# Kernel optimization log

Hardware: AMD Instinct MI355X
Metric: run time of the kernel (lower is better)

Reference implementation:

```python
import math
import jax, jax.numpy as jnp
from jax import lax
import numpy as np

B, HH, WW = 8, 128, 128
N = HH * WW
DIM, NH = 256, 4
HD = DIM // 2 // NH          # 32, per-head dim of the halved channels
CH = DIM // 2                # 128
THETA, MAXSEQ = 10000.0, 4096

# --- static FoPE frequency setup (mirrors RotaryEmbedding.get_inv_freq with fope=True) ---
def _inv_freq():
    rot = 2 * HD                                   # rotary dim = d_model//n_heads = 2*head_dim
    inv = 1.0 / THETA ** (np.arange(0, rot, 2, dtype=np.float64) / rot)
    return inv[inv >= 2.0 * np.pi / MAXSEQ].astype(np.float32)

INV_FREQ = _inv_freq()
D_IN = int(INV_FREQ.shape[0])                      # 23
D_OUT = D_IN if D_IN <= (2 * HD) // 4 else (2 * HD) // 4   # 16


def _coef(key, gain=0.5):
    # xavier_normal_ on (NH, D_IN, D_OUT) + step-eye offset, as in FourierEmbedding.__init__
    fan_in, fan_out = D_IN * D_OUT, NH * D_OUT
    std = gain * math.sqrt(2.0 / (fan_in + fan_out))
    c = std * jax.random.normal(key, (NH, D_IN, D_OUT), jnp.float32)
    step = math.ceil(D_IN / D_OUT)
    eye = np.zeros((NH, D_IN, D_OUT), np.float32)
    for i in range(D_OUT):
        if i * step < D_IN:
            eye[:, i * step, i] = 1.0
    return c + jnp.asarray(eye)


def setup_inputs() -> dict:
    key = jax.random.key(0)
    ks = jax.random.split(key, 10)
    def lin(k, o, i):
        lim = 1.0 / math.sqrt(i)
        return jax.random.uniform(k, (o, i), jnp.float32, -lim, lim)
    return {
        "x": jax.random.normal(ks[0], (B, N, DIM), jnp.float32),
        "Wq": lin(ks[1], CH, DIM), "bq": jnp.zeros((CH,), jnp.float32),
        "Wk": lin(ks[2], CH, DIM), "bk": jnp.zeros((CH,), jnp.float32),
        "Wv": lin(ks[3], CH, DIM), "bv": jnp.zeros((CH,), jnp.float32),
        # Hedgehog maps init as identity
        "Whq": jnp.eye(HD, dtype=jnp.float32), "bhq": jnp.zeros((HD,), jnp.float32),
        "Whk": jnp.eye(HD, dtype=jnp.float32), "bhk": jnp.zeros((HD,), jnp.float32),
        "sin_coef": _coef(ks[4]), "cos_coef": _coef(ks[5]),
        "lepe_w": 0.02 * jax.random.normal(ks[6], (CH, 1, 3, 3), jnp.float32),
        "lepe_b": jnp.zeros((CH,), jnp.float32),
        "temperature": jnp.ones((CH, 1), jnp.float32),
        "Wp": lin(ks[7], DIM, DIM), "bp": jnp.zeros((DIM,), jnp.float32),
        "h": HH, "w": WW,
    }


def _hedgehog(t, W, b):
    # t: [b,h,n,HD] -> [b,h,n,2*HD]
    y = jnp.einsum('bhnd,ed->bhne', t, W) + b
    return jax.nn.softmax(jnp.concatenate([2.0 * y, -2.0 * y], axis=-1), axis=-1)


def _fope(t, sin_coef, cos_coef, n):
    # t: [b,h,n,2*HD]; learnable Fourier rotary
    freqs = jnp.arange(n, dtype=jnp.float32)[:, None] * jnp.asarray(INV_FREQ)[None, :]  # [n,D_IN]
    cs = sin_coef / sin_coef.sum(axis=-2, keepdims=True)
    cc = cos_coef / cos_coef.sum(axis=-2, keepdims=True)
    fs = jnp.einsum('tD,hDd->htd', jnp.sin(freqs), cs)[None]   # [1,h,n,D_OUT]
    fc = jnp.einsum('tD,hDd->htd', jnp.cos(freqs), cc)[None]
    pad = ((0, 0), (0, 0), (0, 0), (0, HD - D_OUT))
    fs = jnp.pad(fs, pad, constant_values=1.0)
    fc = jnp.pad(fc, pad, constant_values=1.0)
    fs = jnp.concatenate([fs, fs], axis=-1)                    # [1,h,n,2*HD]
    fc = jnp.concatenate([fc, fc], axis=-1)
    x1, x2 = t[..., :HD], t[..., HD:]
    rot = jnp.concatenate([-x2, x1], axis=-1)
    return t * fc - rot * fs


def _forward(x, Wq, bq, Wk, bk, Wv, bv, Whq, bhq, Whk, bhk,
             sin_coef, cos_coef, lepe_w, lepe_b, temperature, Wp, bp, h, w):
    b, n, _ = x.shape
    q = x @ Wq.T + bq   # [b,n,CH]
    k = x @ Wk.T + bk
    v = x @ Wv.T + bv

    # ---- spatial brand (Hedgehog linear attention with Fourier rotary) ----
    qh = q.reshape(b, n, NH, HD).swapaxes(1, 2)   # [b,nh,n,HD]
    kh = k.reshape(b, n, NH, HD).swapaxes(1, 2)
    vh = v.reshape(b, n, NH, HD).swapaxes(1, 2)
    qf = _hedgehog(qh, Whq, bhq)                  # [b,nh,n,2HD]
    kf = _hedgehog(kh, Whk, bhk)
    q_fope = _fope(qf, sin_coef, cos_coef, n)
    k_fope = _fope(kf, sin_coef, cos_coef, n)
    kmean = kf.mean(axis=-2, keepdims=True)                       # [b,nh,1,2HD]
    z = 1.0 / (jnp.einsum('bhnd,bhsd->bhns', qf, kmean) + 1e-6)   # [b,nh,n,1]
    s = n ** (-0.5)
    kv = jnp.einsum('bhnd,bhne->bhde', k_fope * s, vh * s)        # [b,nh,2HD,HD]
    xs = jnp.einsum('bhnd,bhde->bhne', q_fope, kv) * z            # [b,nh,n,HD]
    xs = xs.swapaxes(1, 2).reshape(b, n, CH)
    v_img = vh.swapaxes(-1, -2).reshape(b, CH, h, w)
    conv = lax.conv_general_dilated(v_img, lepe_w, (1, 1), 'SAME',
                                    feature_group_count=CH,
                                    dimension_numbers=('NCHW', 'OIHW', 'NCHW'))
    conv = conv + lepe_b[None, :, None, None]
    x_spatial = conv.reshape(b, CH, n).transpose(0, 2, 1) + xs    # [b,n,CH]

    # ---- channel brand (transposed attention over channels) ----
    qc = q.swapaxes(-1, -2)   # [b,CH,n]
    kc = k.swapaxes(-1, -2)
    vc = v.swapaxes(-1, -2)
    qn = qc / jnp.maximum(jnp.linalg.norm(qc, axis=-1, keepdims=True), 1e-12)
    kn = kc / jnp.maximum(jnp.linalg.norm(kc, axis=-1, keepdims=True), 1e-12)
    attn = jax.nn.softmax(jnp.einsum('bcl,bdl->bcd', qn, kn) * temperature, axis=-1)
    x_channel = jnp.einsum('bcd,bdl->bcl', attn, vc).swapaxes(-1, -2)  # [b,n,CH]

    out = jnp.concatenate([x_spatial, x_channel], axis=-1) @ Wp.T + bp  # [b,n,DIM]
    return out, q, k


def reference(x, Wq, bq, Wk, bk, Wv, bv, Whq, bhq, Whk, bhk,
              sin_coef, cos_coef, lepe_w, lepe_b, temperature, Wp, bp, h, w):
    return _forward(x, Wq, bq, Wk, bk, Wv, bv, Whq, bhq, Whk, bhk,
                    sin_coef, cos_coef, lepe_w, lepe_b, temperature, Wp, bp, h, w)
```

## Files before the change

kernel.cpp:

```cpp
#include <hip/hip_runtime.h>
#include <cmath>

#define NB 8
#define NN 16384
#define DIN 23
#define DOUT 16

typedef short bf16x8 __attribute__((ext_vector_type(8)));
typedef float f32x4 __attribute__((ext_vector_type(4)));

__device__ __forceinline__ unsigned short f2bf(float f) {
    unsigned int u = __float_as_uint(f);
    u += 0x7FFFu + ((u >> 16) & 1u);
    return (unsigned short)(u >> 16);
}
__device__ __forceinline__ float bf2f(unsigned short s) {
    return __uint_as_float(((unsigned int)s) << 16);
}
__device__ __forceinline__ float rcpf(float x) { return __builtin_amdgcn_rcpf(x); }

__device__ __forceinline__ bf16x8 cvt8(float4 a, float4 b) {
    bf16x8 r;
    r[0]=(short)f2bf(a.x); r[1]=(short)f2bf(a.y); r[2]=(short)f2bf(a.z); r[3]=(short)f2bf(a.w);
    r[4]=(short)f2bf(b.x); r[5]=(short)f2bf(b.y); r[6]=(short)f2bf(b.z); r[7]=(short)f2bf(b.w);
    return r;
}
__device__ __forceinline__ void red16(f32x4& s) {
    #pragma unroll
    for (int off = 1; off < 16; off <<= 1) {
        s[0] += __shfl_xor(s[0], off); s[1] += __shfl_xor(s[1], off);
        s[2] += __shfl_xor(s[2], off); s[3] += __shfl_xor(s[3], off);
    }
}
__device__ __forceinline__ void red16x2(f32x4& s, f32x4& w) {
    #pragma unroll
    for (int off = 1; off < 16; off <<= 1) {
        s[0] += __shfl_xor(s[0], off); s[1] += __shfl_xor(s[1], off);
        s[2] += __shfl_xor(s[2], off); s[3] += __shfl_xor(s[3], off);
        w[0] += __shfl_xor(w[0], off); w[1] += __shfl_xor(w[1], off);
        w[2] += __shfl_xor(w[2], off); w[3] += __shfl_xor(w[3], off);
    }
}

#define WS_XSPB   ((size_t)0)
#define WS_G      ((size_t)8388608)
#define WS_VB     ((size_t)16777216)
#define WS_XSB    ((size_t)25165824)
#define WS_FS     ((size_t)33554432)
#define WS_INV    ((size_t)35651584)
#define WS_CS     ((size_t)35651648)
#define WS_CC     ((size_t)35653184)
#define WS_WCAT   ((size_t)35654720)
#define WS_BCAT   ((size_t)35703872)
#define WS_KVPART ((size_t)35704256)
#define WS_KMPART ((size_t)37801408)
#define WS_KV     ((size_t)37866944)
#define WS_KMEAN  ((size_t)37932480)
#define WS_QN2    ((size_t)37934528)
#define WS_KN2    ((size_t)37935552)
#define WS_ATTN   ((size_t)38067648)
#define WS_BMATT  ((size_t)38198720)
#define WS_QB     ((size_t)38460864)
#define WS_KB     ((size_t)46849472)

__global__ __launch_bounds__(256) void k_wprep(
    const float* __restrict__ Wq, const float* __restrict__ Wk, const float* __restrict__ Wv,
    const float* __restrict__ bq, const float* __restrict__ bk, const float* __restrict__ bv,
    const float* __restrict__ sc, const float* __restrict__ ccin,
    unsigned short* __restrict__ Wc, float* __restrict__ bcat,
    float* __restrict__ inv, float* __restrict__ cs, float* __restrict__ cc)
{
    int row = blockIdx.x, t = threadIdx.x;
    if (row == 384) {
        if (t >= 64) return;
        if (t < DIN) inv[t] = (float)pow(10000.0, -((double)(2 * t)) / 64.0);
        int h = t >> 4, d = t & 15;
        float ss = 0.f, s2 = 0.f;
        for (int D = 0; D < DIN; ++D) { ss += sc[(h*DIN + D)*DOUT + d]; s2 += ccin[(h*DIN + D)*DOUT + d]; }
        float rs = 1.f / ss, r2 = 1.f / s2;
        for (int D = 0; D < DIN; ++D) {
            cs[(h*DIN + D)*DOUT + d] = sc[(h*DIN + D)*DOUT + d] * rs;
            cc[(h*DIN + D)*DOUT + d] = ccin[(h*DIN + D)*DOUT + d] * r2;
        }
        return;
    }
    const float* W = (row < 128) ? Wq : (row < 256) ? Wk : Wv;
    const float* bb = (row < 128) ? bq : (row < 256) ? bk : bv;
    int r = row & 127;
    Wc[(size_t)row*256 + t] = f2bf(W[(size_t)r*256 + t]);
    if (t == 0) bcat[row] = bb[r];
}

__global__ __launch_bounds__(256) void k_tables(const float* __restrict__ inv, const float* __restrict__ cs,
                                                const float* __restrict__ cc,
                                                unsigned int* __restrict__ fsc)
{
    int t = threadIdx.x;
    int sub = t >> 6, lane = t & 63;
    int tpos = blockIdx.x*4 + sub;
    __shared__ float ssin[4][DIN], scos[4][DIN];
    if (lane < DIN) { float fr = (float)tpos * inv[lane]; ssin[sub][lane] = sinf(fr); scos[sub][lane] = cosf(fr); }
    __syncthreads();
    int h = lane >> 4, d = lane & 15;
    float as = 0.f, ac = 0.f;
    for (int D = 0; D < DIN; ++D) { as += ssin[sub][D]*cs[(h*DIN + D)*DOUT + d]; ac += scos[sub][D]*cc[(h*DIN + D)*DOUT + d]; }
    fsc[((size_t)h*NN + tpos)*16 + d] = ((unsigned int)f2bf(ac) << 16) | (unsigned int)f2bf(as);
}

__global__ __launch_bounds__(512) void k_qkv_mfma(const float* __restrict__ x,
    const unsigned short* __restrict__ Wc, const float* __restrict__ bcat,
    float* __restrict__ q, float* __restrict__ k,
    unsigned short* __restrict__ qb, unsigned short* __restrict__ kb,
    unsigned short* __restrict__ vb)
{
    __shared__ __align__(16) char smem[65536];
    int t = threadIdx.x;
    int lin = blockIdx.x;
    int mtile = (lin & 7)*128 + (lin >> 3);
    int m0 = mtile * 128;
    int wave = t >> 6, lane = t & 63;
    int wm = wave >> 2, wn = wave & 3;
    int lrow = lane & 15, lk = lane >> 4;
    f32x4 acc[4][6];
    #pragma unroll
    for (int i = 0; i < 4; ++i)
        #pragma unroll
        for (int j = 0; j < 6; ++j) acc[i][j] = (f32x4){0.f,0.f,0.f,0.f};

    int am = t >> 4, ak4 = t & 15;
    size_t arow = (size_t)(m0 + am);
    float4 pa[4];
    #pragma unroll
    for (int p = 0; p < 4; ++p)
        pa[p] = *reinterpret_cast<const float4*>(&x[(arow + p*32)*256 + ak4*4]);

    #pragma unroll
    for (int kt = 0; kt < 4; ++kt) {
        int k0 = kt * 64;
        if (kt) __syncthreads();
        #pragma unroll
        for (int p = 0; p < 4; ++p) {
            int m = am + p*32;
            ushort4 b4;
            b4.x = f2bf(pa[p].x); b4.y = f2bf(pa[p].y); b4.z = f2bf(pa[p].z); b4.w = f2bf(pa[p].w);
            int byte = m*128 + ((ak4*8) ^ ((m & 7) << 4));
            *reinterpret_cast<ushort4*>(smem + byte) = b4;
        }
        {
            int n = t >> 3, k8 = t & 7;
            #pragma unroll
            for (int p = 0; p < 6; ++p, n += 64) {
                uint4 u4 = *reinterpret_cast<const uint4*>(&Wc[(size_t)n*256 + k0 + k8*8]);
                int byte = n*128 + ((k8 ^ (n & 7)) << 4);
                *reinterpret_cast<uint4*>(smem + 16384 + byte) = u4;
            }
        }
        if (kt < 3) {
            #pragma unroll
            for (int p = 0; p < 4; ++p)
                pa[p] = *reinterpret_cast<const float4*>(&x[(arow + p*32)*256 + (kt+1)*64 + ak4*4]);
        }
        __syncthreads();
        #pragma unroll
        for (int ks = 0; ks < 2; ++ks) {
            bf16x8 af[4];
            #pragma unroll
            for (int mi = 0; mi < 4; ++mi) {
                int m = wm*64 + mi*16 + lrow;
                int u = (ks*4 + lk) ^ (m & 7);
                af[mi] = *reinterpret_cast<const bf16x8*>(smem + m*128 + u*16);
            }
            #pragma unroll
            for (int ni = 0; ni < 6; ++ni) {
                int n = wn*96 + ni*16 + lrow;
                int u = (ks*4 + lk) ^ (n & 7);
                bf16x8 bfv = *reinterpret_cast<const bf16x8*>(smem + 16384 + n*128 + u*16);
                #pragma unroll
                for (int mi = 0; mi < 4; ++mi)
                    acc[mi][ni] = __builtin_amdgcn_mfma_f32_16x16x32_bf16(af[mi], bfv, acc[mi][ni], 0, 0, 0);
            }
        }
    }
    #pragma unroll
    for (int mi = 0; mi < 4; ++mi) {
        #pragma unroll
        for (int ni = 0; ni < 6; ++ni) {
            int gcol = wn*96 + ni*16 + lrow;
            int c = gcol & 127;
            float bias = bcat[gcol];
            #pragma unroll
            for (int r = 0; r < 4; ++r) {
                size_t grow = (size_t)m0 + wm*64 + mi*16 + lk*4 + r;
                float val = acc[mi][ni][r] + bias;
                if (gcol < 128)      { __builtin_nontemporal_store(val, &q[grow*128 + c]); qb[grow*128 + c] = f2bf(val); }
                else if (gcol < 256) { __builtin_nontemporal_store(val, &k[grow*128 + c]); kb[grow*128 + c] = f2bf(val); }
                else                 vb[grow*128 + c] = f2bf(val);
            }
        }
    }
}

__global__ __launch_bounds__(256) void k_conv(const unsigned short* __restrict__ vb, const float* __restrict__ w,
                                              const float* __restrict__ bias, unsigned short* __restrict__ xspb)
{
    __shared__ float wsmT[9][128];
    __shared__ float bsm[128];
    int t = threadIdx.x;
    for (int i = t; i < 1152; i += 256) wsmT[i % 9][i / 9] = w[i];
    if (t < 128) bsm[t] = bias[t];
    __syncthreads();
    int jj = t >> 4, c8 = (t & 15) * 8;
    int j = blockIdx.x * 16 + jj;
    int i = blockIdx.y, b = blockIdx.z;
    float acc[8];
    #pragma unroll
    for (int l = 0; l < 8; ++l) acc[l] = bsm[c8 + l];
    #pragma unroll
    for (int di = 0; di < 3; ++di) {
        int ii = i + di - 1;
        if (ii < 0 || ii >= 128) continue;
        #pragma unroll
        for (int dj = 0; dj < 3; ++dj) {
            int jx = j + dj - 1;
            if (jx < 0 || jx >= 128) continue;
            uint4 u = *reinterpret_cast<const uint4*>(&vb[((size_t)b*NN + ii*128 + jx)*128 + c8]);
            const unsigned short* us = (const unsigned short*)&u;
            int kk = di*3 + dj;
            #pragma unroll
            for (int l = 0; l < 8; ++l)
                acc[l] += wsmT[kk][c8 + l] * bf2f(us[l]);
        }
    }
    ushort4 r0, r1;
    r0.x = f2bf(acc[0]); r0.y = f2bf(acc[1]); r0.z = f2bf(acc[2]); r0.w = f2bf(acc[3]);
    r1.x = f2bf(acc[4]); r1.y = f2bf(acc[5]); r1.z = f2bf(acc[6]); r1.w = f2bf(acc[7]);
    size_t ob = ((size_t)b*NN + i*128 + j)*128 + c8;
    *reinterpret_cast<ushort4*>(&xspb[ob]) = r0;
    *reinterpret_cast<ushort4*>(&xspb[ob+4]) = r1;
}

__global__ __launch_bounds__(256) void k_featkv(
    const unsigned short* __restrict__ kb, const unsigned short* __restrict__ vb,
    const float* __restrict__ W, const float* __restrict__ bvec,
    const unsigned int* __restrict__ fsc,
    float* __restrict__ kvpart, float* __restrict__ kmpart)
{
    __shared__ __align__(16) char smem[34816];
    __shared__ float kms[4][64];
    int bh = blockIdx.y, b = bh >> 2, h = bh & 3;
    int chunk = blockIdx.x;
    int t = threadIdx.x, w = t >> 6, lane = t & 63;
    int c = lane & 15, g = lane >> 4;
    unsigned short* kfsTw = reinterpret_cast<unsigned short*>(smem) + w*2560;
    unsigned short* vTw   = reinterpret_cast<unsigned short*>(smem + 20480) + w*1280;
    bf16x8 wb[2];
    #pragma unroll
    for (int et = 0; et < 2; ++et) {
        float4 wa = *reinterpret_cast<const float4*>(&W[(c + et*16)*32 + g*8]);
        float4 wb2 = *reinterpret_cast<const float4*>(&W[(c + et*16)*32 + g*8 + 4]);
        wb[et] = cvt8(wa, wb2);
    }
    float bias0 = bvec[c], bias1 = bvec[c + 16];
    f32x4 acc[4][2];
    #pragma unroll
    for (int i = 0; i < 4; ++i) { acc[i][0] = (f32x4){0.f,0.f,0.f,0.f}; acc[i][1] = (f32x4){0.f,0.f,0.f,0.f}; }
    f32x4 km0 = {0.f,0.f,0.f,0.f}, km1 = km0, km2 = km0, km3 = km0;

    for (int rnd = 0; rnd < 4; ++rnd) {
        int p0 = chunk*512 + w*128 + rnd*32;
        {
            uint4 vr0, vr1;
            size_t vbase = ((size_t)(b*NN + p0 + c*2))*128 + h*32 + g*8;
            vr0 = *reinterpret_cast<const uint4*>(&vb[vbase]);
            vr1 = *reinterpret_cast<const uint4*>(&vb[vbase + 128]);
            #pragma unroll
            for (int j = 0; j < 8; ++j) {
                ushort2 pk;
                pk.x = ((const unsigned short*)&vr0)[j];
                pk.y = ((const unsigned short*)&vr1)[j];
                *reinterpret_cast<ushort2*>(&vTw[(g*8 + j)*40 + c*2]) = pk;
            }
        }
        #pragma unroll
        for (int mt = 0; mt < 2; ++mt) {
            int posA = p0 + mt*16 + c;
            bf16x8 af = *reinterpret_cast<const bf16x8*>(&kb[((size_t)(b*NN + posA))*128 + h*32 + g*8]);
            f32x4 z4 = {0.f,0.f,0.f,0.f};
            f32x4 y0 = __builtin_amdgcn_mfma_f32_16x16x32_bf16(af, wb[0], z4, 0, 0, 0);
            f32x4 y1 = __builtin_amdgcn_mfma_f32_16x16x32_bf16(af, wb[1], z4, 0, 0, 0);
            f32x4 el0, eh0, el1, eh1;
            #pragma unroll
            for (int r = 0; r < 4; ++r) {
                float a0 = 2.f*(y0[r] + bias0);
                float a1 = 2.f*(y1[r] + bias1);
                el0[r] = __expf(a0); eh0[r] = __expf(-a0);
                el1[r] = __expf(a1); eh1[r] = __expf(-a1);
            }
            f32x4 s = el0 + eh0 + el1 + eh1;
            red16(s);
            f32x4 rs;
            #pragma unroll
            for (int r = 0; r < 4; ++r) rs[r] = rcpf(s[r]);
            f32x4 klo0 = el0*rs, khi0 = eh0*rs, klo1 = el1*rs, khi1 = eh1*rs;
            km0 += klo0; km1 += khi0; km2 += klo1; km3 += khi1;
            int posC = p0 + mt*16 + g*4;
            ushort4 wlo0, whi0, wlo1, whi1;
            #pragma unroll
            for (int r = 0; r < 4; ++r) {
                unsigned int u = fsc[((size_t)h*NN + posC + r)*16 + c];
                float fsv = bf2f((unsigned short)(u & 0xffffu));
                float fcv = bf2f((unsigned short)(u >> 16));
                ((unsigned short*)&wlo0)[r] = f2bf(klo0[r]*fcv + khi0[r]*fsv);
                ((unsigned short*)&whi0)[r] = f2bf(khi0[r]*fcv - klo0[r]*fsv);
                ((unsigned short*)&wlo1)[r] = f2bf(klo1[r] + khi1[r]);
                ((unsigned short*)&whi1)[r] = f2bf(khi1[r] - klo1[r]);
            }
            int po = mt*16 + g*4;
            *reinterpret_cast<ushort4*>(&kfsTw[(c)*40 + po])      = wlo0;
            *reinterpret_cast<ushort4*>(&kfsTw[(32 + c)*40 + po]) = whi0;
            *reinterpret_cast<ushort4*>(&kfsTw[(16 + c)*40 + po]) = wlo1;
            *reinterpret_cast<ushort4*>(&kfsTw[(48 + c)*40 + po]) = whi1;
        }
        {
            bf16x8 bf0 = *reinterpret_cast<const bf16x8*>(&vTw[(c)*40 + g*8]);
            bf16x8 bf1 = *reinterpret_cast<const bf16x8*>(&vTw[(16 + c)*40 + g*8]);
            #pragma unroll
            for (int mt = 0; mt < 4; ++mt) {
                bf16x8 af2 = *reinterpret_cast<const bf16x8*>(&kfsTw[(mt*16 + c)*40 + g*8]);
                acc[mt][0] = __builtin_amdgcn_mfma_f32_16x16x32_bf16(af2, bf0, acc[mt][0], 0, 0, 0);
                acc[mt][1] = __builtin_amdgcn_mfma_f32_16x16x32_bf16(af2, bf1, acc[mt][1], 0, 0, 0);
            }
        }
    }
    float kv0 = km0[0]+km0[1]+km0[2]+km0[3];
    float kv1 = km1[0]+km1[1]+km1[2]+km1[3];
    float kv2 = km2[0]+km2[1]+km2[2]+km2[3];
    float kv3 = km3[0]+km3[1]+km3[2]+km3[3];
    kv0 += __shfl_xor(kv0, 16); kv0 += __shfl_xor(kv0, 32);
    kv1 += __shfl_xor(kv1, 16); kv1 += __shfl_xor(kv1, 32);
    kv2 += __shfl_xor(kv2, 16); kv2 += __shfl_xor(kv2, 32);
    kv3 += __shfl_xor(kv3, 16); kv3 += __shfl_xor(kv3, 32);
    if (g == 0) {
        kms[w][c] = kv0; kms[w][16 + c] = kv2; kms[w][32 + c] = kv1; kms[w][48 + c] = kv3;
    }
    __syncthreads();
    float* kvred = reinterpret_cast<float*>(smem);
    #pragma unroll
    for (int mt = 0; mt < 4; ++mt)
        #pragma unroll
        for (int nt = 0; nt < 2; ++nt) {
            int d = nt*16 + c;
            *reinterpret_cast<f32x4*>(&kvred[(size_t)(w*32 + d)*68 + mt*16 + g*4]) = acc[mt][nt];
        }
    __syncthreads();
    #pragma unroll
    for (int i = 0; i < 8; ++i) {
        int idx = t*8 + i;
        int f = idx >> 5, d = idx & 31;
        float s2 = kvred[(0*32 + d)*68 + f] + kvred[(1*32 + d)*68 + f]
                 + kvred[(2*32 + d)*68 + f] + kvred[(3*32 + d)*68 + f];
        kvpart[((size_t)(bh*32 + chunk))*2048 + idx] = s2;
    }
    if (t < 64) {
        float s2 = kms[0][t] + kms[1][t] + kms[2][t] + kms[3][t];
        kmpart[(size_t)(bh*32 + chunk)*64 + t] = s2;
    }
}

__global__ __launch_bounds__(256) void k_kvred2(const float* __restrict__ kvpart, const float* __restrict__ kmpart,
                                                unsigned short* __restrict__ kvT, float* __restrict__ kmean)
{
    int bh = blockIdx.x >> 3, part = blockIdx.x & 7;
    int idx = part*256 + threadIdx.x;
    float s = 0.f;
    for (int cidx = 0; cidx < 32; ++cidx) s += kvpart[((size_t)(bh*32 + cidx))*2048 + idx];
    int f = idx >> 5, d = idx & 31;
    kvT[(size_t)bh*2048 + d*64 + f] = f2bf(s * (1.f/16384.f));
    if (part == 0 && threadIdx.x < 64) {
        int tt = threadIdx.x;
        float sm = 0.f;
        for (int cidx = 0; cidx < 32; ++cidx) sm += kmpart[(size_t)(bh*32 + cidx)*64 + tt];
        kmean[bh*64 + tt] = sm * (1.f/16384.f);
    }
}

__global__ __launch_bounds__(256) void k_featxs(
    const unsigned short* __restrict__ qb, const float* __restrict__ W, const float* __restrict__ bvec,
    const unsigned int* __restrict__ fsc, const unsigned short* __restrict__ kvT,
    const float* __restrict__ kmean, const unsigned short* __restrict__ xspb, unsigned short* __restrict__ xsb)
{
    __shared__ __align__(16) unsigned short qfs[4][32][72];
    int bh = blockIdx.y, b = bh >> 2, h = bh & 3;
    int chunk = blockIdx.x;
    int t = threadIdx.x, w = t >> 6, lane = t & 63;
    int c = lane & 15, g = lane >> 4;
    bf16x8 wb[2];
    #pragma unroll
    for (int et = 0; et < 2; ++et) {
        float4 wa = *reinterpret_cast<const float4*>(&W[(c + et*16)*32 + g*8]);
        float4 wb2 = *reinterpret_cast<const float4*>(&W[(c + et*16)*32 + g*8 + 4]);
        wb[et] = cvt8(wa, wb2);
    }
    float bias0 = bvec[c], bias1 = bvec[c + 16];
    float kml0 = kmean[bh*64 + c],      kml1 = kmean[bh*64 + 16 + c];
    float kmh0 = kmean[bh*64 + 32 + c], kmh1 = kmean[bh*64 + 48 + c];
    bf16x8 bkv[2][2];
    #pragma unroll
    for (int nt = 0; nt < 2; ++nt)
        #pragma unroll
        for (int ks = 0; ks < 2; ++ks)
            bkv[nt][ks] = *reinterpret_cast<const bf16x8*>(&kvT[(size_t)bh*2048 + (nt*16 + c)*64 + ks*32 + g*8]);

    for (int rnd = 0; rnd < 2; ++rnd) {
        int p0 = chunk*256 + w*64 + rnd*32;
        #pragma unroll
        for (int mt = 0; mt < 2; ++mt) {
            int posA = p0 + mt*16 + c;
            bf16x8 af = *reinterpret_cast<const bf16x8*>(&qb[((size_t)(b*NN + posA))*128 + h*32 + g*8]);
            f32x4 z4 = {0.f,0.f,0.f,0.f};
            f32x4 y0 = __builtin_amdgcn_mfma_f32_16x16x32_bf16(af, wb[0], z4, 0, 0, 0);
            f32x4 y1 = __builtin_amdgcn_mfma_f32_16x16x32_bf16(af, wb[1], z4, 0, 0, 0);
            f32x4 el0, eh0, el1, eh1;
            #pragma unroll
            for (int r = 0; r < 4; ++r) {
                float a0 = 2.f*(y0[r] + bias0);
                float a1 = 2.f*(y1[r] + bias1);
                el0[r] = __expf(a0); eh0[r] = __expf(-a0);
                el1[r] = __expf(a1); eh1[r] = __expf(-a1);
            }
            f32x4 s = el0 + eh0 + el1 + eh1;
            f32x4 wv = el0*kml0 + eh0*kmh0 + el1*kml1 + eh1*kmh1;
            red16x2(s, wv);
            f32x4 zr;
            #pragma unroll
            for (int r = 0; r < 4; ++r) {
                float rs = rcpf(s[r]);
                float z = rcpf(wv[r]*rs + 1e-6f);
                zr[r] = z*rs;
            }
            int posC = mt*16 + g*4;
            #pragma unroll
            for (int r = 0; r < 4; ++r) {
                unsigned int u = fsc[((size_t)h*NN + p0 + posC + r)*16 + c];
                float fsv = bf2f((unsigned short)(u & 0xffffu));
                float fcv = bf2f((unsigned short)(u >> 16));
                qfs[w][posC + r][c]      = f2bf(zr[r]*(el0[r]*fcv + eh0[r]*fsv));
                qfs[w][posC + r][32 + c] = f2bf(zr[r]*(eh0[r]*fcv - el0[r]*fsv));
                qfs[w][posC + r][16 + c] = f2bf(zr[r]*(el1[r] + eh1[r]));
                qfs[w][posC + r][48 + c] = f2bf(zr[r]*(eh1[r] - el1[r]));
            }
        }
        f32x4 acc[2][2];
        #pragma unroll
        for (int i = 0; i < 2; ++i) { acc[i][0] = (f32x4){0.f,0.f,0.f,0.f}; acc[i][1] = (f32x4){0.f,0.f,0.f,0.f}; }
        #pragma unroll
        for (int ks = 0; ks < 2; ++ks)
            #pragma unroll
            for (int mt = 0; mt < 2; ++mt) {
                bf16x8 af2 = *reinterpret_cast<const bf16x8*>(&qfs[w][mt*16 + c][ks*32 + g*8]);
                acc[mt][0] = __builtin_amdgcn_mfma_f32_16x16x32_bf16(af2, bkv[0][ks], acc[mt][0], 0, 0, 0);
                acc[mt][1] = __builtin_amdgcn_mfma_f32_16x16x32_bf16(af2, bkv[1][ks], acc[mt][1], 0, 0, 0);
            }
        #pragma unroll
        for (int mt = 0; mt < 2; ++mt)
            #pragma unroll
            for (int nt = 0; nt < 2; ++nt) {
                int d = nt*16 + c;
                #pragma unroll
                for (int r = 0; r < 4; ++r) {
                    int pos = p0 + mt*16 + g*4 + r;
                    size_t off = ((size_t)(b*NN + pos))*128 + h*32 + d;
                    xsb[off] = f2bf(bf2f(xspb[off]) + acc[mt][nt][r]);
                }
            }
    }
}

__global__ __launch_bounds__(256) void k_gram(const unsigned short* __restrict__ qb, const unsigned short* __restrict__ kb,
                                              float* __restrict__ G,
                                              float* __restrict__ qn2, float* __restrict__ kn2)
{
    __shared__ unsigned short qTs[128][40];
    __shared__ unsigned short kTs[128][40];
    int kc = blockIdx.x, bb = blockIdx.y;
    int t = threadIdx.x, lane = t & 63;
    int wave = t >> 6, wm = wave >> 1, wn = wave & 1;
    int c = t & 127, lh = t >> 7;
    float qa = 0.f, ka = 0.f;
    f32x4 acc[4][4];
    #pragma unroll
    for (int i = 0; i < 4; ++i)
        #pragma unroll
        for (int j = 0; j < 4; ++j) acc[i][j] = (f32x4){0.f,0.f,0.f,0.f};

    for (int kt = 0; kt < 16; ++kt) {
        __syncthreads();
        #pragma unroll
        for (int i = 0; i < 16; ++i) {
            int l = lh*16 + i;
            size_t pos = (size_t)bb*NN + kc*512 + kt*32 + l;
            unsigned short qu = qb[pos*128 + c];
            unsigned short ku = kb[pos*128 + c];
            float qv = bf2f(qu), kvv = bf2f(ku);
            qa += qv*qv; ka += kvv*kvv;
            qTs[c][l] = qu;
            kTs[c][l] = ku;
        }
        __syncthreads();
        bf16x8 af[4];
        #pragma unroll
        for (int mi = 0; mi < 4; ++mi)
            af[mi] = *reinterpret_cast<const bf16x8*>(&qTs[wm*64 + mi*16 + (lane & 15)][(lane >> 4)*8]);
        #pragma unroll
        for (int ni = 0; ni < 4; ++ni) {
            bf16x8 bfr = *reinterpret_cast<const bf16x8*>(&kTs[wn*64 + ni*16 + (lane & 15)][(lane >> 4)*8]);
            #pragma unroll
            for (int mi = 0; mi < 4; ++mi)
                acc[mi][ni] = __builtin_amdgcn_mfma_f32_16x16x32_bf16(af[mi], bfr, acc[mi][ni], 0, 0, 0);
        }
    }
    #pragma unroll
    for (int mi = 0; mi < 4; ++mi) {
        #pragma unroll
        for (int ni = 0; ni < 4; ++ni) {
            int d = wn*64 + ni*16 + (lane & 15);
            #pragma unroll
            for (int r = 0; r < 4; ++r) {
                int cc = wm*64 + mi*16 + (lane >> 4)*4 + r;
                atomicAdd(&G[(size_t)bb*16384 + (size_t)cc*128 + d], acc[mi][ni][r]);
            }
        }
    }
    atomicAdd(&qn2[bb*128 + c], qa);
    atomicAdd(&kn2[bb*128 + c], ka);
}

__global__ __launch_bounds__(128) void k_attnsm(const float* __restrict__ G, const float* __restrict__ qn2,
    const float* __restrict__ kn2, const float* __restrict__ temp, float* __restrict__ attn)
{
    __shared__ float red[128];
    int row = blockIdx.x;
    int b = row >> 7, c = row & 127;
    int t = threadIdx.x;
    float s0 = G[(size_t)b*16384 + (size_t)c*128 + t];
    float qn = fmaxf(sqrtf(qn2[b*128 + c]), 1e-12f);
    float kn = fmaxf(sqrtf(kn2[b*128 + t]), 1e-12f);
    float val = s0 / (qn*kn) * temp[c];
    red[t] = val; __syncthreads();
    for (int s = 64; s > 0; s >>= 1) { if (t < s) red[t] = fmaxf(red[t], red[t+s]); __syncthreads(); }
    float mm = red[0]; __syncthreads();
    float ev = expf(val - mm);
    red[t] = ev; __syncthreads();
    for (int s = 64; s > 0; s >>= 1) { if (t < s) red[t] += red[t+s]; __syncthreads(); }
    attn[(size_t)row*128 + t] = ev / red[0];
}

__global__ __launch_bounds__(256) void k_bmat(const float* __restrict__ attn, const float* __restrict__ Wp,
                                              unsigned short* __restrict__ BmatT)
{
    int b = blockIdx.y, kk = blockIdx.x, o = threadIdx.x;
    float val;
    if (kk < 128) {
        val = Wp[(size_t)o*256 + kk];
    } else {
        int d = kk - 128;
        __shared__ float a[128];
        if (o < 128) a[o] = attn[((size_t)b*128 + o)*128 + d];
        __syncthreads();
        float acc = 0.f;
        for (int c = 0; c < 128; ++c) acc += a[c] * Wp[(size_t)o*256 + 128 + c];
        val = acc;
    }
    BmatT[((size_t)b*256 + o)*256 + kk] = f2bf(val);
}

__global__ __launch_bounds__(256) void k_out_mfma(const unsigned short* __restrict__ xsb,
    const unsigned short* __restrict__ vb, const unsigned short* __restrict__ BmatT,
    const float* __restrict__ bp, float* __restrict__ out)
{
    __shared__ unsigned short Asm[128*64];
    __shared__ unsigned short Bsm[128*64];
    int t = threadIdx.x;
    int lin = blockIdx.y*2 + blockIdx.x;
    int logical = (lin & 7)*256 + (lin >> 3);
    int ntile = logical & 1;
    int mtile = logical >> 1;
    int m0 = mtile * 128;
    int n0 = ntile * 128;
    int b = mtile >> 7;
    int wave = t >> 6, lane = t & 63;
    int wm = wave >> 1, wn = wave & 1;
    int lrow = lane & 15, lk = lane >> 4;
    f32x4 acc[4][4];
    #pragma unroll
    for (int i = 0; i < 4; ++i)
        #pragma unroll
        for (int j = 0; j < 4; ++j) acc[i][j] = (f32x4){0.f,0.f,0.f,0.f};

    int am = t >> 3, ak8 = t & 7;
    uint4 pa4[4];
    #pragma unroll
    for (int p = 0; p < 4; ++p)
        pa4[p] = *reinterpret_cast<const uint4*>(&xsb[(size_t)(m0 + am + p*32)*128 + ak8*8]);

    #pragma unroll
    for (int kt = 0; kt < 4; ++kt) {
        if (kt) __syncthreads();
        #pragma unroll
        for (int p = 0; p < 4; ++p) {
            int m = am + p*32;
            int byte = m*128 + ((ak8 ^ (m & 7)) << 4);
            *reinterpret_cast<uint4*>(reinterpret_cast<char*>(Asm) + byte) = pa4[p];
        }
        {
            int n = t >> 3, k8 = t & 7;
            #pragma unroll
            for (int p = 0; p < 4; ++p, n += 32) {
                uint4 u4 = *reinterpret_cast<const uint4*>(&BmatT[((size_t)b*256 + n0 + n)*256 + kt*64 + k8*8]);
                int byte = n*128 + ((k8 ^ (n & 7)) << 4);
                *reinterpret_cast<uint4*>(reinterpret_cast<char*>(Bsm) + byte) = u4;
            }
        }
        if (kt < 3) {
            const unsigned short* Asrc = ((kt+1) < 2) ? xsb : vb;
            int ka0 = ((kt+1) & 1) * 64;
            #pragma unroll
            for (int p = 0; p < 4; ++p)
                pa4[p] = *reinterpret_cast<const uint4*>(&Asrc[(size_t)(m0 + am + p*32)*128 + ka0 + ak8*8]);
        }
        __syncthreads();
        #pragma unroll
        for (int ks = 0; ks < 2; ++ks) {
            bf16x8 af[4], bfv[4];
            #pragma unroll
            for (int mi = 0; mi < 4; ++mi) {
                int m = wm*64 + mi*16 + lrow;
                int u = (ks*4 + lk) ^ (m & 7);
                af[mi] = *reinterpret_cast<const bf16x8*>(reinterpret_cast<const char*>(Asm) + m*128 + u*16);
            }
            #pragma unroll
            for (int ni = 0; ni < 4; ++ni) {
                int n = wn*64 + ni*16 + lrow;
                int u = (ks*4 + lk) ^ (n & 7);
                bfv[ni] = *reinterpret_cast<const bf16x8*>(reinterpret_cast<const char*>(Bsm) + n*128 + u*16);
            }
            #pragma unroll
            for (int mi = 0; mi < 4; ++mi)
                #pragma unroll
                for (int ni = 0; ni < 4; ++ni)
                    acc[mi][ni] = __builtin_amdgcn_mfma_f32_16x16x32_bf16(af[mi], bfv[ni], acc[mi][ni], 0, 0, 0);
        }
    }
    #pragma unroll
    for (int mi = 0; mi < 4; ++mi) {
        #pragma unroll
        for (int ni = 0; ni < 4; ++ni) {
            int gcol = n0 + wn*64 + ni*16 + lrow;
            float bias = bp[gcol];
            #pragma unroll
            for (int r = 0; r < 4; ++r) {
                size_t grow = (size_t)m0 + wm*64 + mi*16 + lk*4 + r;
                __builtin_nontemporal_store(acc[mi][ni][r] + bias, &out[grow*256 + gcol]);
            }
        }
    }
}

extern "C" void kernel_launch(void* const* d_in, const int* in_sizes, int n_in,
                              void* d_out, int out_size, void* d_ws, size_t ws_size,
                              hipStream_t stream)
{
    (void)in_sizes; (void)n_in; (void)out_size; (void)ws_size;
    const float* x    = (const float*)d_in[0];
    const float* Wq   = (const float*)d_in[1];
    const float* bq   = (const float*)d_in[2];
    const float* Wk   = (const float*)d_in[3];
    const float* bk   = (const float*)d_in[4];
    const float* Wv   = (const float*)d_in[5];
    const float* bv   = (const float*)d_in[6];
    const float* Whq  = (const float*)d_in[7];
    const float* bhq  = (const float*)d_in[8];
    const float* Whk  = (const float*)d_in[9];
    const float* bhk  = (const float*)d_in[10];
    const float* sinc = (const float*)d_in[11];
    const float* cosc = (const float*)d_in[12];
    const float* lw   = (const float*)d_in[13];
    const float* lb   = (const float*)d_in[14];
    const float* temp = (const float*)d_in[15];
    const float* Wp   = (const float*)d_in[16];
    const float* bp   = (const float*)d_in[17];

    float* out = (float*)d_out;
    float* q   = out + 33554432;
    float* k   = out + 50331648;
    float* ws  = (float*)d_ws;

    unsigned short* xspb = (unsigned short*)(ws + WS_XSPB);
    float* G      = ws + WS_G;
    unsigned short* vbuf = (unsigned short*)(ws + WS_VB);
    unsigned short* xsb  = (unsigned short*)(ws + WS_XSB);
    unsigned int* fsc = (unsigned int*)(ws + WS_FS);
    float* inv    = ws + WS_INV;
    float* cs     = ws + WS_CS;
    float* cc     = ws + WS_CC;
    unsigned short* Wc = (unsigned short*)(ws + WS_WCAT);
    float* bcat   = ws + WS_BCAT;
    float* kvpart = ws + WS_KVPART;
    float* kmpart = ws + WS_KMPART;
    unsigned short* kvT = (unsigned short*)(ws + WS_KV);
    float* kmean  = ws + WS_KMEAN;
    float* qn2    = ws + WS_QN2;
    float* kn2    = ws + WS_KN2;
    float* attn   = ws + WS_ATTN;
    unsigned short* BmatT = (unsigned short*)(ws + WS_BMATT);
    unsigned short* qbuf  = (unsigned short*)(ws + WS_QB);
    unsigned short* kbuf  = (unsigned short*)(ws + WS_KB);

    hipMemsetAsync(qn2, 0, 2048*sizeof(float), stream);
    hipMemsetAsync(G, 0, 131072*sizeof(float), stream);

    k_wprep<<<385, 256, 0, stream>>>(Wq, Wk, Wv, bq, bk, bv, sinc, cosc, Wc, bcat, inv, cs, cc);
    k_tables<<<4096, 256, 0, stream>>>(inv, cs, cc, fsc);
    k_qkv_mfma<<<1024, 512, 0, stream>>>(x, Wc, bcat, q, k, qbuf, kbuf, vbuf);
    k_conv<<<dim3(8, 128, 8), 256, 0, stream>>>(vbuf, lw, lb, xspb);
    k_featkv<<<dim3(32, 32), 256, 0, stream>>>(kbuf, vbuf, Whk, bhk, fsc, kvpart, kmpart);
    k_kvred2<<<256, 256, 0, stream>>>(kvpart, kmpart, kvT, kmean);
    k_featxs<<<dim3(64, 32), 256, 0, stream>>>(qbuf, Whq, bhq, fsc, kvT, kmean, xspb, xsb);
    k_gram<<<dim3(32, 8), 256, 0, stream>>>(qbuf, kbuf, G, qn2, kn2);
    k_attnsm<<<1024, 128, 0, stream>>>(G, qn2, kn2, temp, attn);
    k_bmat<<<dim3(256, 8), 256, 0, stream>>>(attn, Wp, BmatT);
    k_out_mfma<<<dim3(2, 1024), 256, 0, stream>>>(xsb, vbuf, BmatT, bp, out);
}
```

Before: 355.9 us.

## Fold buffer zeroing into weight prep and widen gram kernel split with vector loads

Removes the two memset launches by having extra blocks of k_wprep zero the Gram matrix and norm accumulators. The gram kernel now splits the sequence into 128 chunks instead of 32, raising block count, and loads q/k rows as 16-byte vectors rather than scalar shorts. Per-channel norms are reduced in shared memory before one atomic per channel per block. In exchange, four times as many blocks issue atomics on G, adding atomic traffic.

Result: slower. 385.2 us (+8.3%).

```diff
diff --git a/kernel.cpp b/kernel.cpp
--- a/kernel.cpp
+++ b/kernel.cpp
@@ -68,9 +68,21 @@
     const float* __restrict__ bq, const float* __restrict__ bk, const float* __restrict__ bv,
     const float* __restrict__ sc, const float* __restrict__ ccin,
     unsigned short* __restrict__ Wc, float* __restrict__ bcat,
-    float* __restrict__ inv, float* __restrict__ cs, float* __restrict__ cc)
+    float* __restrict__ inv, float* __restrict__ cs, float* __restrict__ cc,
+    float* __restrict__ G, float* __restrict__ qn2base)
 {
     int row = blockIdx.x, t = threadIdx.x;
+    if (row >= 385) {
+        int z = row - 385;
+        if (z < 128) {
+            f32x4 zr = {0.f,0.f,0.f,0.f};
+            *reinterpret_cast<f32x4*>(&G[(size_t)z*1024 + t*4]) = zr;
+        } else {
+            f32x4 zr = {0.f,0.f,0.f,0.f};
+            *reinterpret_cast<f32x4*>(&qn2base[(size_t)(z-128)*1024 + t*4]) = zr;
+        }
+        return;
+    }
     if (row == 384) {
         if (t >= 64) return;
         if (t < DIN) inv[t] = (float)pow(10000.0, -((double)(2 * t)) / 64.0);
@@ -485,26 +497,31 @@
     int kc = blockIdx.x, bb = blockIdx.y;
     int t = threadIdx.x, lane = t & 63;
     int wave = t >> 6, wm = wave >> 1, wn = wave & 1;
-    int c = t & 127, lh = t >> 7;
-    float qa = 0.f, ka = 0.f;
+    int rl = t >> 4, ch8 = (t & 15) * 8;
+    float qa[8] = {}, ka[8] = {};
     f32x4 acc[4][4];
     #pragma unroll
     for (int i = 0; i < 4; ++i)
         #pragma unroll
         for (int j = 0; j < 4; ++j) acc[i][j] = (f32x4){0.f,0.f,0.f,0.f};
 
-    for (int kt = 0; kt < 16; ++kt) {
+    for (int kt = 0; kt < 4; ++kt) {
         __syncthreads();
         #pragma unroll
-        for (int i = 0; i < 16; ++i) {
-            int l = lh*16 + i;
-            size_t pos = (size_t)bb*NN + kc*512 + kt*32 + l;
-            unsigned short qu = qb[pos*128 + c];
-            unsigned short ku = kb[pos*128 + c];
-            float qv = bf2f(qu), kvv = bf2f(ku);
-            qa += qv*qv; ka += kvv*kvv;
-            qTs[c][l] = qu;
-            kTs[c][l] = ku;
+        for (int p = 0; p < 2; ++p) {
+            int l = rl + p*16;
+            size_t pos = (size_t)bb*NN + kc*128 + kt*32 + l;
+            uint4 qu = *reinterpret_cast<const uint4*>(&qb[pos*128 + ch8]);
+            uint4 ku = *reinterpret_cast<const uint4*>(&kb[pos*128 + ch8]);
+            const unsigned short* qs = (const unsigned short*)&qu;
+            const unsigned short* ks2 = (const unsigned short*)&ku;
+            #pragma unroll
+            for (int j = 0; j < 8; ++j) {
+                float qv = bf2f(qs[j]), kvv = bf2f(ks2[j]);
+                qa[j] += qv*qv; ka[j] += kvv*kvv;
+                qTs[ch8 + j][l] = qs[j];
+                kTs[ch8 + j][l] = ks2[j];
+            }
         }
         __syncthreads();
         bf16x8 af[4];
@@ -518,6 +535,22 @@
             for (int mi = 0; mi < 4; ++mi)
                 acc[mi][ni] = __builtin_amdgcn_mfma_f32_16x16x32_bf16(af[mi], bfr, acc[mi][ni], 0, 0, 0);
         }
+    }
+    __syncthreads();
+    float* redq = reinterpret_cast<float*>(&qTs[0][0]);
+    float* redk = reinterpret_cast<float*>(&kTs[0][0]);
+    #pragma unroll
+    for (int j = 0; j < 8; ++j) {
+        redq[(ch8 + j)*16 + rl] = qa[j];
+        redk[(ch8 + j)*16 + rl] = ka[j];
+    }
+    __syncthreads();
+    if (t < 128) {
+        float sq = 0.f, sk = 0.f;
+        #pragma unroll
+        for (int i = 0; i < 16; ++i) { sq += redq[t*16 + i]; sk += redk[t*16 + i]; }
+        atomicAdd(&qn2[bb*128 + t], sq);
+        atomicAdd(&kn2[bb*128 + t], sk);
     }
     #pragma unroll
     for (int mi = 0; mi < 4; ++mi) {
@@ -531,8 +564,6 @@
             }
         }
     }
-    atomicAdd(&qn2[bb*128 + c], qa);
-    atomicAdd(&kn2[bb*128 + c], ka);
 }
 
 __global__ __launch_bounds__(128) void k_attnsm(const float* __restrict__ G, const float* __restrict__ qn2,
@@ -716,17 +747,14 @@
     unsigned short* qbuf  = (unsigned short*)(ws + WS_QB);
     unsigned short* kbuf  = (unsigned short*)(ws + WS_KB);
 
-    hipMemsetAsync(qn2, 0, 2048*sizeof(float), stream);
-    hipMemsetAsync(G, 0, 131072*sizeof(float), stream);
-
-    k_wprep<<<385, 256, 0, stream>>>(Wq, Wk, Wv, bq, bk, bv, sinc, cosc, Wc, bcat, inv, cs, cc);
+    k_wprep<<<515, 256, 0, stream>>>(Wq, Wk, Wv, bq, bk, bv, sinc, cosc, Wc, bcat, inv, cs, cc, G, qn2);
     k_tables<<<4096, 256, 0, stream>>>(inv, cs, cc, fsc);
     k_qkv_mfma<<<1024, 512, 0, stream>>>(x, Wc, bcat, q, k, qbuf, kbuf, vbuf);
     k_conv<<<dim3(8, 128, 8), 256, 0, stream>>>(vbuf, lw, lb, xspb);
     k_featkv<<<dim3(32, 32), 256, 0, stream>>>(kbuf, vbuf, Whk, bhk, fsc, kvpart, kmpart);
     k_kvred2<<<256, 256, 0, stream>>>(kvpart, kmpart, kvT, kmean);
     k_featxs<<<dim3(64, 32), 256, 0, stream>>>(qbuf, Whq, bhq, fsc, kvT, kmean, xspb, xsb);
-    k_gram<<<dim3(32, 8), 256, 0, stream>>>(qbuf, kbuf, G, qn2, kn2);
+    k_gram<<<dim3(128, 8), 256, 0, stream>>>(qbuf, kbuf, G, qn2, kn2);
     k_attnsm<<<1024, 128, 0, stream>>>(G, qn2, kn2, temp, attn);
     k_bmat<<<dim3(256, 8), 256, 0, stream>>>(attn, Wp, BmatT);
     k_out_mfma<<<dim3(2, 1024), 256, 0, stream>>>(xsb, vbuf, BmatT, bp, out);
```
